# Performance work log

Hardware: AMD Instinct MI355X
Metric: run time of the kernel (lower is better)

The kernel has to match this reference:

```python
import jax, jax.numpy as jnp
import numpy as np

TAU = 0.05
SK_ITERS = 20


def spmm(index, value, m, dense):
    # sparse (m x m) COO @ dense (m x f)
    row, col = index[0], index[1]
    return jax.ops.segment_sum(value[:, None] * dense[col], row, num_segments=m)


def mlp2(x, W1, b1, W2, b2):
    h = jax.nn.relu(x @ W1 + b1)
    return jax.nn.relu(h @ W2 + b2)


def sinkhorn(s):
    # log-domain Sinkhorn, row norm on even iters, col norm on odd iters
    log_s = s / TAU
    for i in range(SK_ITERS):
        axis = 2 if i % 2 == 0 else 1
        log_s = log_s - jax.nn.logsumexp(log_s, axis=axis, keepdims=True)
    return jnp.exp(log_s)


def setup_inputs() -> dict:
    key = jax.random.key(0)
    ks = jax.random.split(key, 16)
    n1, n2 = 256, 256
    n = n1 * n2
    nnzK, nnzA = 1048576, 524288
    in_f, out_f, sk_ch = 64, 63, 1
    inp = {}
    inp['K_value'] = jax.random.normal(ks[0], (nnzK,), jnp.float32)
    inp['index'] = jax.random.randint(ks[1], (2, nnzK), 0, n)
    inp['normed_A_value'] = jax.random.uniform(ks[2], (nnzA,), jnp.float32)
    inp['A_index'] = jax.random.randint(ks[3], (2, nnzA), 0, n)
    inp['x'] = jax.random.normal(ks[4], (1, n, in_f), jnp.float32)
    # n_func
    inp['Wn1'] = jax.random.normal(ks[5], (in_f, out_f), jnp.float32) / np.sqrt(in_f)
    inp['bn1'] = jnp.zeros((out_f,), jnp.float32)
    inp['Wn2'] = jax.random.normal(ks[6], (out_f, out_f), jnp.float32) / np.sqrt(out_f)
    inp['bn2'] = jnp.zeros((out_f,), jnp.float32)
    # n_self_func
    inp['Ws1'] = jax.random.normal(ks[7], (in_f, out_f), jnp.float32) / np.sqrt(in_f)
    inp['bs1'] = jnp.zeros((out_f,), jnp.float32)
    inp['Ws2'] = jax.random.normal(ks[8], (out_f, out_f), jnp.float32) / np.sqrt(out_f)
    inp['bs2'] = jnp.zeros((out_f,), jnp.float32)
    # classifier
    inp['Wc'] = jax.random.normal(ks[9], (out_f, sk_ch), jnp.float32) / np.sqrt(out_f)
    inp['bc'] = jnp.zeros((sk_ch,), jnp.float32)
    inp['n1'] = n1
    inp['n2'] = n2
    return inp


def reference(K_value, index, normed_A_value, A_index, x,
              Wn1, bn1, Wn2, bn2, Ws1, bs1, Ws2, bs2, Wc, bc, n1, n2):
    n = n1 * n2
    sk_ch = Wc.shape[1]
    x1 = mlp2(x[0], Wn1, bn1, Wn2, bn2)                 # (n, out_f)
    Wx = spmm(index, K_value, n, x1)                    # (n, out_f)
    x2 = spmm(A_index, normed_A_value, n, Wx)[None]     # (1, n, out_f)
    x2 = x2 + mlp2(x, Ws1, bs1, Ws2, bs2)
    x3 = x2 @ Wc + bc                                   # (1, n, sk_ch)
    # (1,n,sk) -> (sk, n2, n1) -> (sk, n1, n2)
    x4 = jnp.transpose(x3, (0, 2, 1)).reshape(sk_ch, n2, n1)
    x4 = jnp.transpose(x4, (0, 2, 1))
    x5 = jnp.transpose(sinkhorn(x4), (0, 2, 1))         # (sk, n2, n1)
    x6 = jnp.transpose(x5.reshape(1, sk_ch, n), (0, 2, 1))  # (1, n, sk)
    return jnp.concatenate((x2, x6), axis=-1)
```

## Files before the change

### kernel.cpp

```cpp
#include <hip/hip_runtime.h>
#include <hip/hip_bf16.h>

#define FI 64
#define FO 63
#define FP 64
#define NZPW 8
#define INV_TAU 20.0f
#define LOG2E 1.4426950408889634f
#define CHUNK 4096
#define SCAP 12288

__device__ __forceinline__ float fexp2(float x) {
    float y; asm("v_exp_f32 %0, %1" : "=v"(y) : "v"(x)); return y;
}
__device__ __forceinline__ float flog2(float x) {
    float y; asm("v_log_f32 %0, %1" : "=v"(y) : "v"(x)); return y;
}

__global__ __launch_bounds__(256) void k_mlp_n(
    const float* __restrict__ x,
    const float* __restrict__ W1, const float* __restrict__ b1,
    const float* __restrict__ W2, const float* __restrict__ b2,
    float* __restrict__ x1p, int n)
{
    int t = blockIdx.x * 256 + threadIdx.x;
    if (t >= n) return;
    const float* xr = x + (size_t)t * FI;

    float h[FO];
#pragma unroll
    for (int j = 0; j < FO; ++j) h[j] = b1[j];
#pragma unroll 1
    for (int ii = 0; ii < FI; ii += 4) {
        float4 xq = *(const float4*)(xr + ii);
#pragma unroll
        for (int j = 0; j < FO; ++j) h[j] = fmaf(xq.x, W1[(ii+0)*FO+j], h[j]);
#pragma unroll
        for (int j = 0; j < FO; ++j) h[j] = fmaf(xq.y, W1[(ii+1)*FO+j], h[j]);
#pragma unroll
        for (int j = 0; j < FO; ++j) h[j] = fmaf(xq.z, W1[(ii+2)*FO+j], h[j]);
#pragma unroll
        for (int j = 0; j < FO; ++j) h[j] = fmaf(xq.w, W1[(ii+3)*FO+j], h[j]);
    }
#pragma unroll
    for (int j = 0; j < FO; ++j) h[j] = fmaxf(h[j], 0.f);

    float o[FO];
#pragma unroll
    for (int j = 0; j < FO; ++j) o[j] = b2[j];
#pragma unroll 1
    for (int i = 0; i < FO; ++i) {
        float hi = h[i];
#pragma unroll
        for (int j = 0; j < FO; ++j) o[j] = fmaf(hi, W2[i*FO+j], o[j]);
    }

    float* dst = x1p + (size_t)t * FP;
#pragma unroll
    for (int c = 0; c < 15; ++c) {
        float4 w;
        w.x = fmaxf(o[4*c+0], 0.f);
        w.y = fmaxf(o[4*c+1], 0.f);
        w.z = fmaxf(o[4*c+2], 0.f);
        w.w = fmaxf(o[4*c+3], 0.f);
        ((float4*)dst)[c] = w;
    }
    {
        float4 w;
        w.x = fmaxf(o[60], 0.f);
        w.y = fmaxf(o[61], 0.f);
        w.z = fmaxf(o[62], 0.f);
        w.w = 0.f;
        ((float4*)dst)[15] = w;
    }
}

__global__ __launch_bounds__(256) void k_hist256(
    const int* __restrict__ rowsK, const int* __restrict__ rowsA,
    int* __restrict__ cntK, int* __restrict__ cntA, int nnzK, int nnzA)
{
    __shared__ int h[512];
    int tid = threadIdx.x;
    h[tid] = 0; h[tid + 256] = 0;
    __syncthreads();
    int i = blockIdx.x * 256 + tid;
    int stride = gridDim.x * 256;
    int total = nnzK + nnzA;
    for (; i < total; i += stride) {
        if (i < nnzK) atomicAdd(&h[rowsK[i] >> 8], 1);
        else          atomicAdd(&h[256 + (rowsA[i - nnzK] >> 8)], 1);
    }
    __syncthreads();
    if (h[tid])       atomicAdd(&cntK[tid], h[tid]);
    if (h[tid + 256]) atomicAdd(&cntA[tid], h[tid + 256]);
}

__global__ __launch_bounds__(256) void k_scan256(
    const int* __restrict__ cntK, const int* __restrict__ cntA,
    int* __restrict__ bstartK, int* __restrict__ gcurK,
    int* __restrict__ bstartA, int* __restrict__ gcurA)
{
    __shared__ int tmp[256];
    int t = threadIdx.x;
    int c = cntK[t];
    tmp[t] = c; __syncthreads();
#pragma unroll 1
    for (int off = 1; off < 256; off <<= 1) {
        int v = (t >= off) ? tmp[t - off] : 0;
        __syncthreads();
        tmp[t] += v;
        __syncthreads();
    }
    bstartK[t + 1] = tmp[t];
    gcurK[t] = tmp[t] - c;
    if (t == 0) bstartK[0] = 0;
    __syncthreads();
    c = cntA[t];
    tmp[t] = c; __syncthreads();
#pragma unroll 1
    for (int off = 1; off < 256; off <<= 1) {
        int v = (t >= off) ? tmp[t - off] : 0;
        __syncthreads();
        tmp[t] += v;
        __syncthreads();
    }
    bstartA[t + 1] = tmp[t];
    gcurA[t] = tmp[t] - c;
    if (t == 0) bstartA[0] = 0;
}

__global__ __launch_bounds__(256) void kb_bucket(
    const int* __restrict__ rows, const int* __restrict__ cols,
    const float* __restrict__ val, int* __restrict__ gcur,
    int2* __restrict__ sdat, int nnz)
{
    __shared__ int cnt[256], loff[256], cnt2[256], shiftv[256];
    __shared__ int sm_meta[CHUNK];
    __shared__ float sm_val[CHUNK];
    __shared__ unsigned char sm_bid[CHUNK];
    int tid = threadIdx.x;
    int i0 = blockIdx.x * CHUNK;
    int i1 = min(i0 + CHUNK, nnz);
    int m = i1 - i0;

    cnt[tid] = 0; cnt2[tid] = 0;
    __syncthreads();
#pragma unroll 1
    for (int i = i0 + tid; i < i1; i += 256)
        atomicAdd(&cnt[rows[i] >> 8], 1);
    __syncthreads();
    loff[tid] = cnt[tid];
    __syncthreads();
#pragma unroll 1
    for (int off = 1; off < 256; off <<= 1) {
        int v = (tid >= off) ? loff[tid - off] : 0;
        __syncthreads();
        loff[tid] += v;
        __syncthreads();
    }
    int excl = loff[tid] - cnt[tid];
    __syncthreads();
    loff[tid] = excl;
    int gb = cnt[tid] ? atomicAdd(&gcur[tid], cnt[tid]) : 0;
    shiftv[tid] = gb - excl;
    __syncthreads();
#pragma unroll 1
    for (int i = i0 + tid; i < i1; i += 256) {
        int r = rows[i];
        int b = r >> 8;
        int s = loff[b] + atomicAdd(&cnt2[b], 1);
        sm_meta[s] = cols[i] | ((r & 255) << 16);
        sm_val[s]  = val[i];
        sm_bid[s]  = (unsigned char)b;
    }
    __syncthreads();
#pragma unroll 1
    for (int s = tid; s < m; s += 256) {
        int b = sm_bid[s];
        sdat[shiftv[b] + s] = make_int2(sm_meta[s], __float_as_int(sm_val[s]));
    }
}

__global__ __launch_bounds__(256) void kb_sort(
    const int* __restrict__ bstart, int2* __restrict__ sdat,
    int* __restrict__ ptr, int2* __restrict__ scratch)
{
    __shared__ int cnt[256], off[256], cur[256];
    __shared__ int2 stage[SCAP];
    int tid = threadIdx.x;
    int b = blockIdx.x;
    int s = bstart[b], e = bstart[b + 1];
    int m = e - s;
    cnt[tid] = 0;
    __syncthreads();
    bool fits = (m <= SCAP);
    if (fits) {
#pragma unroll 1
        for (int i = tid; i < m; i += 256) {
            int2 d = sdat[s + i];
            stage[i] = d;
            atomicAdd(&cnt[(d.x >> 16) & 255], 1);
        }
    } else {
#pragma unroll 1
        for (int i = tid; i < m; i += 256) {
            int2 d = sdat[s + i];
            scratch[s + i] = d;
            atomicAdd(&cnt[(d.x >> 16) & 255], 1);
        }
    }
    __syncthreads();
    int c = cnt[tid];
    off[tid] = c;
    __syncthreads();
#pragma unroll 1
    for (int o = 1; o < 256; o <<= 1) {
        int v = (tid >= o) ? off[tid - o] : 0;
        __syncthreads();
        off[tid] += v;
        __syncthreads();
    }
    ptr[b * 256 + tid] = s + off[tid];
    cur[tid] = off[tid] - c;
    __syncthreads();
    if (fits) {
#pragma unroll 1
        for (int i = tid; i < m; i += 256) {
            int2 d = stage[i];
            int p = atomicAdd(&cur[(d.x >> 16) & 255], 1);
            sdat[s + p] = d;
        }
    } else {
        __threadfence();
        __syncthreads();
#pragma unroll 1
        for (int i = tid; i < m; i += 256) {
            int2 d = scratch[s + i];
            int p = atomicAdd(&cur[(d.x >> 16) & 255], 1);
            sdat[s + p] = d;
        }
    }
}

__global__ __launch_bounds__(256) void kb_gather(
    const int* __restrict__ ptr, const int2* __restrict__ sdat,
    const float* __restrict__ xin,
    float* __restrict__ out, int n)
{
    int r = blockIdx.x * 4 + (threadIdx.x >> 6);
    int lane = threadIdx.x & 63;
    if (r >= n) return;
    int s = (r == 0) ? 0 : ptr[r - 1];
    int e = ptr[r];
    float acc = 0.f;
    int k = s;
#pragma unroll 1
    for (; k + 3 < e; k += 4) {
        int2 d0 = sdat[k],     d1 = sdat[k + 1];
        int2 d2 = sdat[k + 2], d3 = sdat[k + 3];
        float x0 = xin[((d0.x & 0xFFFF) << 6) + lane];
        float x1 = xin[((d1.x & 0xFFFF) << 6) + lane];
        float x2 = xin[((d2.x & 0xFFFF) << 6) + lane];
        float x3 = xin[((d3.x & 0xFFFF) << 6) + lane];
        acc = fmaf(__int_as_float(d0.y), x0, acc);
        acc = fmaf(__int_as_float(d1.y), x1, acc);
        acc = fmaf(__int_as_float(d2.y), x2, acc);
        acc = fmaf(__int_as_float(d3.y), x3, acc);
    }
#pragma unroll 1
    for (; k < e; ++k) {
        int2 d0 = sdat[k];
        acc = fmaf(__int_as_float(d0.y), xin[((d0.x & 0xFFFF) << 6) + lane], acc);
    }
    out[((size_t)r << 6) + lane] = acc;
}

__global__ __launch_bounds__(256) void k_hist(
    const int* __restrict__ rows, int* __restrict__ cnt, int nnz)
{
    int i = blockIdx.x * 256 + threadIdx.x;
    int stride = gridDim.x * 256;
    for (; i < nnz; i += stride) atomicAdd(&cnt[rows[i]], 1);
}

__global__ __launch_bounds__(1024) void k_scan2(
    int* __restrict__ ptrK, int* __restrict__ ptrA)
{
    __shared__ int tot[1024];
    int* ptr = (blockIdx.x == 0) ? ptrK : ptrA;
    int t = threadIdx.x;
    int4* p4 = (int4*)(ptr + t * 64);
    int sum = 0;
#pragma unroll 1
    for (int q = 0; q < 16; ++q) {
        int4 b = p4[q];
        sum += b.x + b.y + b.z + b.w;
    }
    tot[t] = sum;
    __syncthreads();
#pragma unroll 1
    for (int off = 1; off < 1024; off <<= 1) {
        int v2 = 0;
        if (t >= off) v2 = tot[t - off];
        __syncthreads();
        if (t >= off) tot[t] += v2;
        __syncthreads();
    }
    int off = (t == 0) ? 0 : tot[t - 1];
#pragma unroll 1
    for (int q = 0; q < 16; ++q) {
        int4 b = p4[q];
        int4 w;
        w.x = off; off += b.x;
        w.y = off; off += b.y;
        w.z = off; off += b.z;
        w.w = off; off += b.w;
        p4[q] = w;
    }
}

__global__ __launch_bounds__(256) void k_scatter(
    const int* __restrict__ rows, const int* __restrict__ cols,
    const float* __restrict__ val, int* __restrict__ ptr,
    int2* __restrict__ sdat, int nnz)
{
    int i = blockIdx.x * 256 + threadIdx.x;
    int stride = gridDim.x * 256;
    for (; i < nnz; i += stride) {
        int p = atomicAdd(&ptr[rows[i]], 1);
        sdat[p] = make_int2(cols[i], __float_as_int(val[i]));
    }
}

__global__ __launch_bounds__(256) void k_gather(
    const int* __restrict__ ptr, const int2* __restrict__ sdat,
    const float* __restrict__ xin,
    float* __restrict__ out, int n)
{
    int r = blockIdx.x * 4 + (threadIdx.x >> 6);
    int lane = threadIdx.x & 63;
    if (r >= n) return;
    int s = (r == 0) ? 0 : ptr[r - 1];
    int e = ptr[r];
    float acc = 0.f;
    int k = s;
#pragma unroll 1
    for (; k + 3 < e; k += 4) {
        int2 d0 = sdat[k],     d1 = sdat[k + 1];
        int2 d2 = sdat[k + 2], d3 = sdat[k + 3];
        float x0 = xin[((size_t)d0.x << 6) + lane];
        float x1 = xin[((size_t)d1.x << 6) + lane];
        float x2 = xin[((size_t)d2.x << 6) + lane];
        float x3 = xin[((size_t)d3.x << 6) + lane];
        acc = fmaf(__int_as_float(d0.y), x0, acc);
        acc = fmaf(__int_as_float(d1.y), x1, acc);
        acc = fmaf(__int_as_float(d2.y), x2, acc);
        acc = fmaf(__int_as_float(d3.y), x3, acc);
    }
#pragma unroll 1
    for (; k < e; ++k) {
        int2 d0 = sdat[k];
        acc = fmaf(__int_as_float(d0.y), xin[((size_t)d0.x << 6) + lane], acc);
    }
    out[((size_t)r << 6) + lane] = acc;
}

__global__ __launch_bounds__(256) void k_spmm(
    const int* __restrict__ rows, const int* __restrict__ cols,
    const float* __restrict__ val, const float* __restrict__ xin,
    float* __restrict__ acc, int nnz)
{
    int wave = blockIdx.x * 4 + (threadIdx.x >> 6);
    int lane = threadIdx.x & 63;
    int e0 = wave * NZPW;
#pragma unroll 1
    for (int k = 0; k < NZPW; ++k) {
        int e = e0 + k;
        if (e >= nnz) break;
        int r = rows[e];
        int c = cols[e];
        float v = val[e];
        float xv = xin[((size_t)c << 6) + lane];
        unsafeAtomicAdd(&acc[((size_t)r << 6) + lane], v * xv);
    }
}

__global__ __launch_bounds__(256) void k_combine(
    const float* __restrict__ x,
    const float* __restrict__ W1, const float* __restrict__ b1,
    const float* __restrict__ W2, const float* __restrict__ b2,
    const float* __restrict__ Wc, const float* __restrict__ bcp,
    const float* __restrict__ x2b,
    float* __restrict__ out, float* __restrict__ x3, int n)
{
    int t = blockIdx.x * 256 + threadIdx.x;
    if (t >= n) return;
    const float* xr = x + (size_t)t * FI;

    float h[FO];
#pragma unroll
    for (int j = 0; j < FO; ++j) h[j] = b1[j];
#pragma unroll 1
    for (int ii = 0; ii < FI; ii += 4) {
        float4 xq = *(const float4*)(xr + ii);
#pragma unroll
        for (int j = 0; j < FO; ++j) h[j] = fmaf(xq.x, W1[(ii+0)*FO+j], h[j]);
#pragma unroll
        for (int j = 0; j < FO; ++j) h[j] = fmaf(xq.y, W1[(ii+1)*FO+j], h[j]);
#pragma unroll
        for (int j = 0; j < FO; ++j) h[j] = fmaf(xq.z, W1[(ii+2)*FO+j], h[j]);
#pragma unroll
        for (int j = 0; j < FO; ++j) h[j] = fmaf(xq.w, W1[(ii+3)*FO+j], h[j]);
    }
#pragma unroll
    for (int j = 0; j < FO; ++j) h[j] = fmaxf(h[j], 0.f);

    float o[FO];
#pragma unroll
    for (int j = 0; j < FO; ++j) o[j] = b2[j];
#pragma unroll 1
    for (int i = 0; i < FO; ++i) {
        float hi = h[i];
#pragma unroll
        for (int j = 0; j < FO; ++j) o[j] = fmaf(hi, W2[i*FO+j], o[j]);
    }

    const float4* q4 = (const float4*)(x2b + (size_t)t * FP);
    float4* dst = (float4*)(out + (size_t)t * FP);
    float dot = 0.f;
#pragma unroll
    for (int c = 0; c < 15; ++c) {
        float4 q = q4[c];
        float4 w;
        w.x = q.x + fmaxf(o[4*c+0], 0.f);
        w.y = q.y + fmaxf(o[4*c+1], 0.f);
        w.z = q.z + fmaxf(o[4*c+2], 0.f);
        w.w = q.w + fmaxf(o[4*c+3], 0.f);
        dot = fmaf(w.x, Wc[4*c+0], dot);
        dot = fmaf(w.y, Wc[4*c+1], dot);
        dot = fmaf(w.z, Wc[4*c+2], dot);
        dot = fmaf(w.w, Wc[4*c+3], dot);
        dst[c] = w;
    }
    {
        float4 q = q4[15];
        float4 w;
        w.x = q.x + fmaxf(o[60], 0.f);
        w.y = q.y + fmaxf(o[61], 0.f);
        w.z = q.z + fmaxf(o[62], 0.f);
        w.w = 0.f;
        dot = fmaf(w.x, Wc[60], dot);
        dot = fmaf(w.y, Wc[61], dot);
        dot = fmaf(w.z, Wc[62], dot);
        dst[15] = w;
    }
    x3[t] = dot + bcp[0];
}

#define SKP 332
__global__ __launch_bounds__(1024) __attribute__((amdgpu_waves_per_eu(4, 4)))
void k_sinkhorn(const float* __restrict__ x3, float* __restrict__ out)
{
    __shared__ float pm[32][SKP];
    __shared__ float ps[32][SKP];
    __shared__ float Rl[256];
    __shared__ float Cl[256];
    const int tid = threadIdx.x;
    const int ta = tid >> 5, tb = tid & 31;
    const int line4 = tid >> 2, sub = tid & 3;

    float u[8][8];
#pragma unroll
    for (int i = 0; i < 8; ++i) {
        const float4* src = (const float4*)(x3 + (ta*8 + i)*256 + tb*8);
        float4 a0 = src[0], a1 = src[1];
        const float sc = INV_TAU * LOG2E;
        u[i][0] = a0.x * sc; u[i][1] = a0.y * sc;
        u[i][2] = a0.z * sc; u[i][3] = a0.w * sc;
        u[i][4] = a1.x * sc; u[i][5] = a1.y * sc;
        u[i][6] = a1.z * sc; u[i][7] = a1.w * sc;
    }
    if (tid < 256) { Rl[tid] = 0.f; Cl[tid] = 0.f; }
    __syncthreads();

#pragma unroll 1
    for (int it = 0; it < 2; ++it) {
        const bool even = (it & 1) == 0;
        float sm[8], ss[8];
        if (even) {
            float r[8];
#pragma unroll
            for (int i = 0; i < 8; ++i) r[i] = Rl[ta*8 + i];
#pragma unroll
            for (int j = 0; j < 8; ++j) {
                float m = u[0][j] - r[0];
#pragma unroll
                for (int i = 1; i < 8; ++i) m = fmaxf(m, u[i][j] - r[i]);
                float s0 = 0.f, s1 = 0.f;
#pragma unroll
                for (int i = 0; i < 8; i += 2) {
                    s0 += fexp2(u[i][j] - r[i] - m);
                    s1 += fexp2(u[i+1][j] - r[i+1] - m);
                }
                sm[j] = m; ss[j] = s0 + s1;
            }
        } else {
            float c[8];
#pragma unroll
            for (int j = 0; j < 8; ++j) c[j] = Cl[tb*8 + j];
#pragma unroll
            for (int i = 0; i < 8; ++i) {
                float m = u[i][0] - c[0];
#pragma unroll
                for (int j = 1; j < 8; ++j) m = fmaxf(m, u[i][j] - c[j]);
                float s0 = 0.f, s1 = 0.f;
#pragma unroll
                for (int j = 0; j < 8; j += 2) {
                    s0 += fexp2(u[i][j] - c[j] - m);
                    s1 += fexp2(u[i][j+1] - c[j+1] - m);
                }
                sm[i] = m; ss[i] = s0 + s1;
            }
        }
        {
            float* mrow = even ? &pm[ta][tb*8] : &pm[tb][ta*8];
            float* srow = even ? &ps[ta][tb*8] : &ps[tb][ta*8];
            ((float4*)mrow)[0] = make_float4(sm[0], sm[1], sm[2], sm[3]);
            ((float4*)mrow)[1] = make_float4(sm[4], sm[5], sm[6], sm[7]);
            ((float4*)srow)[0] = make_float4(ss[0], ss[1], ss[2], ss[3]);
            ((float4*)srow)[1] = make_float4(ss[4], ss[5], ss[6], ss[7]);
        }
        __syncthreads();
        float M = pm[sub*8][line4];
        float S = ps[sub*8][line4];
#pragma unroll
        for (int k = 1; k < 8; ++k) {
            float m2 = pm[sub*8 + k][line4];
            float s2 = ps[sub*8 + k][line4];
            float nm = fmaxf(M, m2);
            S = S * fexp2(M - nm) + s2 * fexp2(m2 - nm);
            M = nm;
        }
#pragma unroll
        for (int d = 1; d <= 2; d <<= 1) {
            float m2 = __shfl_xor(M, d);
            float s2 = __shfl_xor(S, d);
            float nm = fmaxf(M, m2);
            S = S * fexp2(M - nm) + s2 * fexp2(m2 - nm);
            M = nm;
        }
        if (sub == 0) {
            float l = M + flog2(S);
            if (even) Cl[line4] = l; else Rl[line4] = l;
        }
        __syncthreads();
    }

#pragma unroll 1
    for (int it = 2; it < 20; ++it) {
        const bool even = (it & 1) == 0;
        float r[8], c[8], ss[8];
#pragma unroll
        for (int i = 0; i < 8; ++i) r[i] = Rl[ta*8 + i];
#pragma unroll
        for (int j = 0; j < 8; ++j) c[j] = Cl[tb*8 + j];
        if (even) {
#pragma unroll
            for (int j = 0; j < 8; ++j) {
                float s0 = 0.f, s1 = 0.f;
#pragma unroll
                for (int i = 0; i < 8; i += 2) {
                    s0 += fexp2(u[i][j] - r[i] - c[j]);
                    s1 += fexp2(u[i+1][j] - r[i+1] - c[j]);
                }
                ss[j] = s0 + s1;
            }
        } else {
#pragma unroll
            for (int i = 0; i < 8; ++i) {
                float s0 = 0.f, s1 = 0.f;
#pragma unroll
                for (int j = 0; j < 8; j += 2) {
                    s0 += fexp2(u[i][j] - c[j] - r[i]);
                    s1 += fexp2(u[i][j+1] - c[j+1] - r[i]);
                }
                ss[i] = s0 + s1;
            }
        }
        {
            float* srow = even ? &ps[ta][tb*8] : &ps[tb][ta*8];
            ((float4*)srow)[0] = make_float4(ss[0], ss[1], ss[2], ss[3]);
            ((float4*)srow)[1] = make_float4(ss[4], ss[5], ss[6], ss[7]);
        }
        __syncthreads();
        float S = 0.f;
#pragma unroll
        for (int k = 0; k < 8; ++k) S += ps[sub*8 + k][line4];
        S += __shfl_xor(S, 1);
        S += __shfl_xor(S, 2);
        if (sub == 0) {
            float d = flog2(S);
            if (even) Cl[line4] += d; else Rl[line4] += d;
        }
        __syncthreads();
    }

    float r[8], c[8];
#pragma unroll
    for (int i = 0; i < 8; ++i) r[i] = Rl[ta*8 + i];
#pragma unroll
    for (int j = 0; j < 8; ++j) c[j] = Cl[tb*8 + j];
#pragma unroll
    for (int i = 0; i < 8; ++i) {
        int a = ta*8 + i;
#pragma unroll
        for (int j = 0; j < 8; ++j) {
            out[((size_t)(a*256 + tb*8 + j) << 6) + 63] =
                fexp2(u[i][j] - r[i] - c[j]);
        }
    }
}

extern "C" void kernel_launch(void* const* d_in, const int* in_sizes, int n_in,
                              void* d_out, int out_size, void* d_ws, size_t ws_size,
                              hipStream_t stream)
{
    const float* K_value = (const float*)d_in[0];
    const int*   K_index = (const int*)d_in[1];
    const float* A_value = (const float*)d_in[2];
    const int*   A_index = (const int*)d_in[3];
    const float* x   = (const float*)d_in[4];
    const float* Wn1 = (const float*)d_in[5];
    const float* bn1 = (const float*)d_in[6];
    const float* Wn2 = (const float*)d_in[7];
    const float* bn2 = (const float*)d_in[8];
    const float* Ws1 = (const float*)d_in[9];
    const float* bs1 = (const float*)d_in[10];
    const float* Ws2 = (const float*)d_in[11];
    const float* bs2 = (const float*)d_in[12];
    const float* Wc  = (const float*)d_in[13];
    const float* bc  = (const float*)d_in[14];

    int nnzK = in_sizes[0];
    int nnzA = in_sizes[2];
    int n    = in_sizes[4] / FI;

    const int* rowsK = K_index;  const int* colsK = K_index + nnzK;
    const int* rowsA = A_index;  const int* colsA = A_index + nnzA;

    float* outf = (float*)d_out;
    char*  ws   = (char*)d_ws;
    float* bufA = (float*)ws;
    float* x3   = bufA + (size_t)n * FP;
    int*   tbl  = (int*)x3;
    int*   cntK = tbl;          int* cntA = tbl + 256;
    int*   bstK = tbl + 512;    int* gcrK = tbl + 772;
    int*   bstA = tbl + 1032;   int* gcrA = tbl + 1292;
    int*   ptrKf = (int*)(x3 + n);
    int*   ptrAf = ptrKf + n;
    int2*  sdatK = (int2*)(ptrAf + n);
    int2*  sdatA = sdatK + nnzK;

    size_t need1 = ((size_t)n * FP + 3 * (size_t)n) * 4 + ((size_t)nnzK + nnzA) * 8;
    size_t need2 = ((size_t)n * FP + 2 * (size_t)n) * 4 + (size_t)nnzK * 8;

    k_mlp_n<<<(n + 255) / 256, 256, 0, stream>>>(x, Wn1, bn1, Wn2, bn2, bufA, n);

    if (ws_size >= need1 && n == 65536 && nnzK <= (1 << 24) && nnzA <= (1 << 24)) {
        (void)hipMemsetAsync(cntK, 0, 512 * 4, stream);
        k_hist256<<<512, 256, 0, stream>>>(rowsK, rowsA, cntK, cntA, nnzK, nnzA);
        k_scan256<<<1, 256, 0, stream>>>(cntK, cntA, bstK, gcrK, bstA, gcrA);
        kb_bucket<<<(nnzK + CHUNK - 1) / CHUNK, 256, 0, stream>>>(
            rowsK, colsK, K_value, gcrK, sdatK, nnzK);
        kb_bucket<<<(nnzA + CHUNK - 1) / CHUNK, 256, 0, stream>>>(
            rowsA, colsA, A_value, gcrA, sdatA, nnzA);
        kb_sort<<<256, 256, 0, stream>>>(bstK, sdatK, ptrKf, (int2*)outf);
        kb_sort<<<256, 256, 0, stream>>>(bstA, sdatA, ptrAf, (int2*)outf);
        kb_gather<<<(n + 3) / 4, 256, 0, stream>>>(ptrKf, sdatK, bufA, outf, n);
        kb_gather<<<(n + 3) / 4, 256, 0, stream>>>(ptrAf, sdatA, outf, bufA, n);
    } else if (ws_size >= need2 && n == 65536) {
        int* ptrK = (int*)(x3 + n);
        int2* sdat2 = (int2*)(ptrK + n);
        (void)hipMemsetAsync(ptrK, 0, (size_t)n * 4, stream);
        k_hist<<<2048, 256, 0, stream>>>(rowsK, ptrK, nnzK);
        k_scan2<<<1, 1024, 0, stream>>>(ptrK, ptrK);
        k_scatter<<<2048, 256, 0, stream>>>(rowsK, colsK, K_value, ptrK, sdat2, nnzK);
        k_gather<<<(n + 3) / 4, 256, 0, stream>>>(ptrK, sdat2, bufA, outf, n);
        (void)hipMemsetAsync(ptrK, 0, (size_t)n * 4, stream);
        k_hist<<<2048, 256, 0, stream>>>(rowsA, ptrK, nnzA);
        k_scan2<<<1, 1024, 0, stream>>>(ptrK, ptrK);
        k_scatter<<<2048, 256, 0, stream>>>(rowsA, colsA, A_value, ptrK, sdat2, nnzA);
        k_gather<<<(n + 3) / 4, 256, 0, stream>>>(ptrK, sdat2, outf, bufA, n);
    } else {
        (void)hipMemsetAsync(outf, 0, (size_t)n * FP * 4, stream);
        int blocks1 = (nnzK + 4 * NZPW - 1) / (4 * NZPW);
        k_spmm<<<blocks1, 256, 0, stream>>>(rowsK, colsK, K_value, bufA, outf, nnzK);
        (void)hipMemsetAsync(bufA, 0, (size_t)n * FP * 4, stream);
        int blocks2 = (nnzA + 4 * NZPW - 1) / (4 * NZPW);
        k_spmm<<<blocks2, 256, 0, stream>>>(rowsA, colsA, A_value, outf, bufA, nnzA);
    }

    k_combine<<<(n + 255) / 256, 256, 0, stream>>>(x, Ws1, bs1, Ws2, bs2, Wc, bc,
                                                   bufA, outf, x3, n);
    k_sinkhorn<<<1, 1024, 0, stream>>>(x3, outf);
}
```

Measured before the change: 388.2 us.

## Run late Sinkhorn iterations in linear domain with reciprocal scaling

```diff
diff --git a/kernel.cpp b/kernel.cpp
--- a/kernel.cpp
+++ b/kernel.cpp
@@ -15,6 +15,9 @@
 }
 __device__ __forceinline__ float flog2(float x) {
     float y; asm("v_log_f32 %0, %1" : "=v"(y) : "v"(x)); return y;
+}
+__device__ __forceinline__ float frcp(float x) {
+    float y; asm("v_rcp_f32 %0, %1" : "=v"(y) : "v"(x)); return y;
 }
 
 __global__ __launch_bounds__(256) void k_mlp_n(
@@ -465,6 +468,7 @@
     __shared__ float ps[32][SKP];
     __shared__ float Rl[256];
     __shared__ float Cl[256];
+    __shared__ float Fl[256];
     const int tid = threadIdx.x;
     const int ta = tid >> 5, tb = tid & 31;
     const int line4 = tid >> 2, sub = tid & 3;
@@ -556,67 +560,84 @@
         __syncthreads();
     }
 
+    {
+        float r[8], c[8], sc8[8];
+#pragma unroll
+        for (int i = 0; i < 8; ++i) r[i] = Rl[ta*8 + i];
+#pragma unroll
+        for (int j = 0; j < 8; ++j) { c[j] = Cl[tb*8 + j]; sc8[j] = 0.f; }
+#pragma unroll
+        for (int i = 0; i < 8; ++i) {
+#pragma unroll
+            for (int j = 0; j < 8; ++j) {
+                u[i][j] = fexp2(u[i][j] - r[i] - c[j]);
+                sc8[j] += u[i][j];
+            }
+        }
+        float* srow = &ps[ta][tb*8];
+        ((float4*)srow)[0] = make_float4(sc8[0], sc8[1], sc8[2], sc8[3]);
+        ((float4*)srow)[1] = make_float4(sc8[4], sc8[5], sc8[6], sc8[7]);
+    }
+    __syncthreads();
+
 #pragma unroll 1
     for (int it = 2; it < 20; ++it) {
         const bool even = (it & 1) == 0;
-        float r[8], c[8], ss[8];
-#pragma unroll
-        for (int i = 0; i < 8; ++i) r[i] = Rl[ta*8 + i];
-#pragma unroll
-        for (int j = 0; j < 8; ++j) c[j] = Cl[tb*8 + j];
-        if (even) {
-#pragma unroll
-            for (int j = 0; j < 8; ++j) {
-                float s0 = 0.f, s1 = 0.f;
-#pragma unroll
-                for (int i = 0; i < 8; i += 2) {
-                    s0 += fexp2(u[i][j] - r[i] - c[j]);
-                    s1 += fexp2(u[i+1][j] - r[i+1] - c[j]);
-                }
-                ss[j] = s0 + s1;
-            }
-        } else {
-#pragma unroll
-            for (int i = 0; i < 8; ++i) {
-                float s0 = 0.f, s1 = 0.f;
-#pragma unroll
-                for (int j = 0; j < 8; j += 2) {
-                    s0 += fexp2(u[i][j] - c[j] - r[i]);
-                    s1 += fexp2(u[i][j+1] - c[j+1] - r[i]);
-                }
-                ss[i] = s0 + s1;
-            }
-        }
-        {
-            float* srow = even ? &ps[ta][tb*8] : &ps[tb][ta*8];
-            ((float4*)srow)[0] = make_float4(ss[0], ss[1], ss[2], ss[3]);
-            ((float4*)srow)[1] = make_float4(ss[4], ss[5], ss[6], ss[7]);
-        }
-        __syncthreads();
         float S = 0.f;
 #pragma unroll
         for (int k = 0; k < 8; ++k) S += ps[sub*8 + k][line4];
         S += __shfl_xor(S, 1);
         S += __shfl_xor(S, 2);
-        if (sub == 0) {
-            float d = flog2(S);
-            if (even) Cl[line4] += d; else Rl[line4] += d;
-        }
-        __syncthreads();
-    }
-
-    float r[8], c[8];
-#pragma unroll
-    for (int i = 0; i < 8; ++i) r[i] = Rl[ta*8 + i];
-#pragma unroll
-    for (int j = 0; j < 8; ++j) c[j] = Cl[tb*8 + j];
+        if (sub == 0) Fl[line4] = frcp(S);
+        __syncthreads();
+        if (even) {
+            float f[8], sr[8];
+#pragma unroll
+            for (int j = 0; j < 8; ++j) f[j] = Fl[tb*8 + j];
+#pragma unroll
+            for (int i = 0; i < 8; ++i) sr[i] = 0.f;
+#pragma unroll
+            for (int i = 0; i < 8; ++i) {
+#pragma unroll
+                for (int j = 0; j < 8; ++j) {
+                    u[i][j] *= f[j];
+                    sr[i] += u[i][j];
+                }
+            }
+            if (it < 19) {
+                float* srow = &ps[tb][ta*8];
+                ((float4*)srow)[0] = make_float4(sr[0], sr[1], sr[2], sr[3]);
+                ((float4*)srow)[1] = make_float4(sr[4], sr[5], sr[6], sr[7]);
+            }
+        } else {
+            float f[8], sc8[8];
+#pragma unroll
+            for (int i = 0; i < 8; ++i) f[i] = Fl[ta*8 + i];
+#pragma unroll
+            for (int j = 0; j < 8; ++j) sc8[j] = 0.f;
+#pragma unroll
+            for (int i = 0; i < 8; ++i) {
+#pragma unroll
+                for (int j = 0; j < 8; ++j) {
+                    u[i][j] *= f[i];
+                    sc8[j] += u[i][j];
+                }
+            }
+            if (it < 19) {
+                float* srow = &ps[ta][tb*8];
+                ((float4*)srow)[0] = make_float4(sc8[0], sc8[1], sc8[2], sc8[3]);
+                ((float4*)srow)[1] = make_float4(sc8[4], sc8[5], sc8[6], sc8[7]);
+            }
+        }
+        __syncthreads();
+    }
+
 #pragma unroll
     for (int i = 0; i < 8; ++i) {
         int a = ta*8 + i;
 #pragma unroll
         for (int j = 0; j < 8; ++j) {
-            out[((size_t)(a*256 + tb*8 + j) << 6) + 63] =
-                fexp2(u[i][j] - r[i] - c[j]);
+            out[((size_t)(a*256 + tb*8 + j) << 6) + 63] = u[i][j];
         }
     }
 }
```

After: 401.3 us. 1.03x slower.

## Remap Sinkhorn so each wave owns 16 full rows with shuffle reductions

Applied to the files above, without the earlier changes.

```diff
diff --git a/kernel.cpp b/kernel.cpp
--- a/kernel.cpp
+++ b/kernel.cpp
@@ -457,166 +457,121 @@
     x3[t] = dot + bcp[0];
 }
 
-#define SKP 332
 __global__ __launch_bounds__(1024) __attribute__((amdgpu_waves_per_eu(4, 4)))
 void k_sinkhorn(const float* __restrict__ x3, float* __restrict__ out)
 {
-    __shared__ float pm[32][SKP];
-    __shared__ float ps[32][SKP];
-    __shared__ float Rl[256];
+    __shared__ float pm[16][264];
+    __shared__ float ps[16][264];
     __shared__ float Cl[256];
+    __shared__ float ldspad[12800];
     const int tid = threadIdx.x;
-    const int ta = tid >> 5, tb = tid & 31;
-    const int line4 = tid >> 2, sub = tid & 3;
-
-    float u[8][8];
-#pragma unroll
-    for (int i = 0; i < 8; ++i) {
-        const float4* src = (const float4*)(x3 + (ta*8 + i)*256 + tb*8);
-        float4 a0 = src[0], a1 = src[1];
-        const float sc = INV_TAU * LOG2E;
-        u[i][0] = a0.x * sc; u[i][1] = a0.y * sc;
-        u[i][2] = a0.z * sc; u[i][3] = a0.w * sc;
-        u[i][4] = a1.x * sc; u[i][5] = a1.y * sc;
-        u[i][6] = a1.z * sc; u[i][7] = a1.w * sc;
-    }
-    if (tid < 256) { Rl[tid] = 0.f; Cl[tid] = 0.f; }
-    __syncthreads();
-
-#pragma unroll 1
-    for (int it = 0; it < 2; ++it) {
-        const bool even = (it & 1) == 0;
-        float sm[8], ss[8];
-        if (even) {
-            float r[8];
-#pragma unroll
-            for (int i = 0; i < 8; ++i) r[i] = Rl[ta*8 + i];
-#pragma unroll
-            for (int j = 0; j < 8; ++j) {
-                float m = u[0][j] - r[0];
-#pragma unroll
-                for (int i = 1; i < 8; ++i) m = fmaxf(m, u[i][j] - r[i]);
-                float s0 = 0.f, s1 = 0.f;
-#pragma unroll
-                for (int i = 0; i < 8; i += 2) {
-                    s0 += fexp2(u[i][j] - r[i] - m);
-                    s1 += fexp2(u[i+1][j] - r[i+1] - m);
-                }
-                sm[j] = m; ss[j] = s0 + s1;
+    const int w = tid >> 6;
+    const int l = tid & 63;
+
+    float u[16][4];
+    float R[16];
+    const float sc = INV_TAU * LOG2E;
+#pragma unroll
+    for (int i = 0; i < 16; ++i) {
+        float4 a0 = *(const float4*)(x3 + (w*16 + i)*256 + l*4);
+        u[i][0] = a0.x*sc; u[i][1] = a0.y*sc; u[i][2] = a0.z*sc; u[i][3] = a0.w*sc;
+        R[i] = 0.f;
+    }
+    if (tid < 256) Cl[tid] = 0.f;
+    if (__float_as_int(x3[0]) == 0x7f7f7f7f) ldspad[tid] = 0.f;
+    __syncthreads();
+
+    {
+        float sm[4], ss[4];
+#pragma unroll
+        for (int j = 0; j < 4; ++j) {
+            float m = u[0][j];
+#pragma unroll
+            for (int i = 1; i < 16; ++i) m = fmaxf(m, u[i][j]);
+            float s = 0.f;
+#pragma unroll
+            for (int i = 0; i < 16; ++i) s += fexp2(u[i][j] - m);
+            sm[j] = m; ss[j] = s;
+        }
+        *(float4*)&pm[w][l*4] = make_float4(sm[0], sm[1], sm[2], sm[3]);
+        *(float4*)&ps[w][l*4] = make_float4(ss[0], ss[1], ss[2], ss[3]);
+        __syncthreads();
+        if (tid < 256) {
+            float M = pm[0][tid], S = ps[0][tid];
+#pragma unroll
+            for (int k2 = 1; k2 < 16; ++k2) {
+                float m2 = pm[k2][tid], s2 = ps[k2][tid];
+                float nm = fmaxf(M, m2);
+                S = S * fexp2(M - nm) + s2 * fexp2(m2 - nm);
+                M = nm;
             }
+            Cl[tid] = M + flog2(S);
+        }
+        __syncthreads();
+    }
+
+    {
+        float c0 = Cl[l*4+0], c1 = Cl[l*4+1], c2 = Cl[l*4+2], c3 = Cl[l*4+3];
+#pragma unroll
+        for (int i = 0; i < 16; ++i) {
+            float t0 = u[i][0]-c0, t1 = u[i][1]-c1;
+            float t2 = u[i][2]-c2, t3 = u[i][3]-c3;
+            float m = fmaxf(fmaxf(t0, t1), fmaxf(t2, t3));
+#pragma unroll
+            for (int d = 1; d < 64; d <<= 1) m = fmaxf(m, __shfl_xor(m, d));
+            float s = fexp2(t0-m) + fexp2(t1-m) + fexp2(t2-m) + fexp2(t3-m);
+#pragma unroll
+            for (int d = 1; d < 64; d <<= 1) s += __shfl_xor(s, d);
+            R[i] = m + flog2(s);
+        }
+    }
+
+#pragma unroll 1
+    for (int it = 2; it < 20; ++it) {
+        float c0 = Cl[l*4+0], c1 = Cl[l*4+1], c2 = Cl[l*4+2], c3 = Cl[l*4+3];
+        if ((it & 1) == 0) {
+            float s0 = 0.f, s1 = 0.f, s2 = 0.f, s3 = 0.f;
+#pragma unroll
+            for (int i = 0; i < 16; ++i) {
+                float ri = R[i];
+                s0 += fexp2(u[i][0] - ri - c0);
+                s1 += fexp2(u[i][1] - ri - c1);
+                s2 += fexp2(u[i][2] - ri - c2);
+                s3 += fexp2(u[i][3] - ri - c3);
+            }
+            *(float4*)&ps[w][l*4] = make_float4(s0, s1, s2, s3);
+            __syncthreads();
+            if (tid < 256) {
+                float S = ps[0][tid];
+#pragma unroll
+                for (int k2 = 1; k2 < 16; ++k2) S += ps[k2][tid];
+                Cl[tid] += flog2(S);
+            }
+            __syncthreads();
         } else {
-            float c[8];
-#pragma unroll
-            for (int j = 0; j < 8; ++j) c[j] = Cl[tb*8 + j];
-#pragma unroll
-            for (int i = 0; i < 8; ++i) {
-                float m = u[i][0] - c[0];
-#pragma unroll
-                for (int j = 1; j < 8; ++j) m = fmaxf(m, u[i][j] - c[j]);
-                float s0 = 0.f, s1 = 0.f;
-#pragma unroll
-                for (int j = 0; j < 8; j += 2) {
-                    s0 += fexp2(u[i][j] - c[j] - m);
-                    s1 += fexp2(u[i][j+1] - c[j+1] - m);
-                }
-                sm[i] = m; ss[i] = s0 + s1;
+#pragma unroll
+            for (int i = 0; i < 16; ++i) {
+                float ri = R[i];
+                float s = fexp2(u[i][0]-c0-ri) + fexp2(u[i][1]-c1-ri)
+                        + fexp2(u[i][2]-c2-ri) + fexp2(u[i][3]-c3-ri);
+#pragma unroll
+                for (int d = 1; d < 64; d <<= 1) s += __shfl_xor(s, d);
+                R[i] += flog2(s);
             }
         }
-        {
-            float* mrow = even ? &pm[ta][tb*8] : &pm[tb][ta*8];
-            float* srow = even ? &ps[ta][tb*8] : &ps[tb][ta*8];
-            ((float4*)mrow)[0] = make_float4(sm[0], sm[1], sm[2], sm[3]);
-            ((float4*)mrow)[1] = make_float4(sm[4], sm[5], sm[6], sm[7]);
-            ((float4*)srow)[0] = make_float4(ss[0], ss[1], ss[2], ss[3]);
-            ((float4*)srow)[1] = make_float4(ss[4], ss[5], ss[6], ss[7]);
-        }
-        __syncthreads();
-        float M = pm[sub*8][line4];
-        float S = ps[sub*8][line4];
-#pragma unroll
-        for (int k = 1; k < 8; ++k) {
-            float m2 = pm[sub*8 + k][line4];
-            float s2 = ps[sub*8 + k][line4];
-            float nm = fmaxf(M, m2);
-            S = S * fexp2(M - nm) + s2 * fexp2(m2 - nm);
-            M = nm;
-        }
-#pragma unroll
-        for (int d = 1; d <= 2; d <<= 1) {
-            float m2 = __shfl_xor(M, d);
-            float s2 = __shfl_xor(S, d);
-            float nm = fmaxf(M, m2);
-            S = S * fexp2(M - nm) + s2 * fexp2(m2 - nm);
-            M = nm;
-        }
-        if (sub == 0) {
-            float l = M + flog2(S);
-            if (even) Cl[line4] = l; else Rl[line4] = l;
-        }
-        __syncthreads();
-    }
-
-#pragma unroll 1
-    for (int it = 2; it < 20; ++it) {
-        const bool even = (it & 1) == 0;
-        float r[8], c[8], ss[8];
-#pragma unroll
-        for (int i = 0; i < 8; ++i) r[i] = Rl[ta*8 + i];
-#pragma unroll
-        for (int j = 0; j < 8; ++j) c[j] = Cl[tb*8 + j];
-        if (even) {
-#pragma unroll
-            for (int j = 0; j < 8; ++j) {
-                float s0 = 0.f, s1 = 0.f;
-#pragma unroll
-                for (int i = 0; i < 8; i += 2) {
-                    s0 += fexp2(u[i][j] - r[i] - c[j]);
-                    s1 += fexp2(u[i+1][j] - r[i+1] - c[j]);
-                }
-                ss[j] = s0 + s1;
-            }
-        } else {
-#pragma unroll
-            for (int i = 0; i < 8; ++i) {
-                float s0 = 0.f, s1 = 0.f;
-#pragma unroll
-                for (int j = 0; j < 8; j += 2) {
-                    s0 += fexp2(u[i][j] - c[j] - r[i]);
-                    s1 += fexp2(u[i][j+1] - c[j+1] - r[i]);
-                }
-                ss[i] = s0 + s1;
-            }
-        }
-        {
-            float* srow = even ? &ps[ta][tb*8] : &ps[tb][ta*8];
-            ((float4*)srow)[0] = make_float4(ss[0], ss[1], ss[2], ss[3]);
-            ((float4*)srow)[1] = make_float4(ss[4], ss[5], ss[6], ss[7]);
-        }
-        __syncthreads();
-        float S = 0.f;
-#pragma unroll
-        for (int k = 0; k < 8; ++k) S += ps[sub*8 + k][line4];
-        S += __shfl_xor(S, 1);
-        S += __shfl_xor(S, 2);
-        if (sub == 0) {
-            float d = flog2(S);
-            if (even) Cl[line4] += d; else Rl[line4] += d;
-        }
-        __syncthreads();
-    }
-
-    float r[8], c[8];
-#pragma unroll
-    for (int i = 0; i < 8; ++i) r[i] = Rl[ta*8 + i];
-#pragma unroll
-    for (int j = 0; j < 8; ++j) c[j] = Cl[tb*8 + j];
-#pragma unroll
-    for (int i = 0; i < 8; ++i) {
-        int a = ta*8 + i;
-#pragma unroll
-        for (int j = 0; j < 8; ++j) {
-            out[((size_t)(a*256 + tb*8 + j) << 6) + 63] =
-                fexp2(u[i][j] - r[i] - c[j]);
+    }
+
+    {
+        float c0 = Cl[l*4+0], c1 = Cl[l*4+1], c2 = Cl[l*4+2], c3 = Cl[l*4+3];
+#pragma unroll
+        for (int i = 0; i < 16; ++i) {
+            int a = w*16 + i;
+            size_t base = ((size_t)(a*256 + l*4) << 6) + 63;
+            float ri = R[i];
+            out[base]       = fexp2(u[i][0] - ri - c0);
+            out[base + 64]  = fexp2(u[i][1] - ri - c1);
+            out[base + 128] = fexp2(u[i][2] - ri - c2);
+            out[base + 192] = fexp2(u[i][3] - ri - c3);
         }
     }
 }
```

After: 402.6 us. 1.04x slower.
